# Optimization experiments

Measured on AMD Instinct MI355X. Metric: run time of the kernel, lower is better.

## Reference

```python
import jax, jax.numpy as jnp
import numpy as np

B, V, N, IN_F, HEADS, OUT_F = 4, 4, 1000, 64, 4, 32
D = HEADS * OUT_F  # 128, concat=True
E = 64000
NEG_SLOPE = 0.2


def setup_inputs() -> dict:
    key = jax.random.key(0)
    ks = jax.random.split(key, 8)
    x = jax.random.normal(ks[0], (B, V, N, IN_F), jnp.float32)
    edge_index = jax.random.randint(ks[1], (2, E), 0, B * N, dtype=jnp.int64)
    W = jax.random.normal(ks[2], (HEADS * OUT_F, IN_F), jnp.float32) / np.sqrt(IN_F)
    att = jax.random.normal(ks[3], (1, HEADS, 2 * OUT_F), jnp.float32) * 0.1
    in_proj_w = jax.random.normal(ks[4], (3 * D, D), jnp.float32) / np.sqrt(D)
    in_proj_b = jnp.zeros((3 * D,), jnp.float32)
    out_proj_w = jax.random.normal(ks[5], (D, D), jnp.float32) / np.sqrt(D)
    out_proj_b = jnp.zeros((D,), jnp.float32)
    bias = jnp.zeros((D,), jnp.float32)
    return dict(x=x, W=W, att=att, in_proj_w=in_proj_w, in_proj_b=in_proj_b,
                out_proj_w=out_proj_w, out_proj_b=out_proj_b, bias=bias,
                edge_index=edge_index)


def reference(x, W, att, in_proj_w, in_proj_b, out_proj_w, out_proj_b, bias, edge_index):
    Bx, Vx, Nx, _ = x.shape
    Ntot = Bx * Nx
    # intra-view GAT: shared W across views
    h = jnp.einsum('bvni,oi->bvno', x, W).reshape(Bx, Vx, Nx, HEADS, OUT_F)
    # block-diagonal placement: h_full[b*V+v, b*N:(b+1)*N] = h[b,v]
    ib = jnp.arange(Bx)
    hf = jnp.zeros((Bx, Vx, Bx, Nx, HEADS, OUT_F), x.dtype).at[ib, :, ib].set(h)
    h_full = hf.reshape(Bx * Vx, Ntot, HEADS, OUT_F)
    # add self loops
    loops = jnp.arange(Ntot, dtype=edge_index.dtype)
    src = jnp.concatenate([edge_index[0], loops])
    dst = jnp.concatenate([edge_index[1], loops])
    # attention scores (faithful to source: flatten h_full over (B*V, Ntot) and
    # index with raw node ids, i.e. gathers from block 0 only)
    h_flat = h_full.reshape(Bx * Vx * Ntot, HEADS, OUT_F)
    h_cat = jnp.concatenate([h_flat[src], h_flat[dst]], axis=-1)  # [Etot, H, 2*OUT]
    att_in = jax.nn.leaky_relu(h_cat, NEG_SLOPE)
    scores = jnp.sum(att * att_in, axis=-1)  # [Etot, HEADS]
    # per-destination segment softmax
    seg_max = jax.ops.segment_max(scores, dst, num_segments=Ntot)
    seg_max = jax.lax.stop_gradient(jnp.where(jnp.isfinite(seg_max), seg_max, 0.0))
    ex = jnp.exp(scores - seg_max[dst])
    denom = jax.ops.segment_sum(ex, dst, num_segments=Ntot)
    alpha = ex / (denom[dst] + 1e-16)  # [Etot, HEADS]
    # scatter-add aggregation, broadcast over B*V rows
    msgs = h_full[:, src] * alpha[None, :, :, None]  # [B*V, Etot, H, OUT]
    out_full = jnp.zeros_like(h_full).at[:, dst].add(msgs)
    # extract each graph's own node block
    out = out_full.reshape(Bx, Vx, Bx, Nx, HEADS, OUT_F)[ib, :, ib]  # [B,V,N,H,OUT]
    h_gat = out.reshape(Bx, Vx, Nx, HEADS * OUT_F)  # concat heads
    # inter-view mixing: MHA over the V axis per node
    seq = h_gat.transpose(0, 2, 1, 3).reshape(Bx * Nx, Vx, D)
    q, k, v = jnp.split(seq @ in_proj_w.T + in_proj_b, 3, axis=-1)
    hd = D // HEADS
    sp = lambda t: t.reshape(Bx * Nx, Vx, HEADS, hd).transpose(0, 2, 1, 3)
    q, k, v = sp(q), sp(k), sp(v)
    aw = jax.nn.softmax(jnp.einsum('bhqd,bhkd->bhqk', q, k) / jnp.sqrt(jnp.asarray(hd, x.dtype)), axis=-1)
    ao = jnp.einsum('bhqk,bhkd->bhqd', aw, v).transpose(0, 2, 1, 3).reshape(Bx * Nx, Vx, D)
    mixed = ao @ out_proj_w.T + out_proj_b
    h_mixed = mixed.reshape(Bx, Nx, Vx, D).transpose(0, 2, 1, 3)  # [B,V,N,D]
    return h_mixed + bias
```

## Files before the change

kernel.cpp:

```cpp
#include <hip/hip_runtime.h>

#define NN 1000
#define HEADS_ 4
#define DM 128
#define EE 64000
#define NTOT 4000
#define ETOT 68000
#define CAP 48
#define EB 34

template <int K, int SCORE, int REMAP>
__device__ void gemm_tile(int mi, int ni,
                          const float* __restrict__ A, const float* __restrict__ Wt,
                          const float* __restrict__ b1, const float* __restrict__ b2,
                          float* __restrict__ C, int N,
                          const float* __restrict__ att,
                          float* __restrict__ ssrc, float* __restrict__ sdst) {
  __shared__ float As[128 * 64];
  __shared__ float Bs[64 * 64];
  int tid = threadIdx.x;
  int m0 = mi * 128, n0 = ni * 64;
  int tx = tid & 15, ty = tid >> 4;
  const float4* A4 = (const float4*)A;
  const float4* W4 = (const float4*)Wt;
  float acc[8][4] = {};

  for (int c = 0; c < K / 64; ++c) {
    __syncthreads();
    {
      int q = tid & 15;
      int r0 = tid >> 4;
#pragma unroll
      for (int p = 0; p < 8; ++p) {
        int r = r0 + p * 16;
        float4 v = A4[(size_t)(m0 + r) * (K / 4) + c * 16 + q];
        *(float4*)&As[r * 64 + ((q ^ ((r >> 2) & 15)) << 2)] = v;
      }
#pragma unroll
      for (int p = 0; p < 4; ++p) {
        int r = r0 + p * 16;
        float4 v = W4[(size_t)(n0 + r) * (K / 4) + c * 16 + q];
        *(float4*)&Bs[r * 64 + ((q ^ ((r >> 2) & 15)) << 2)] = v;
      }
    }
    __syncthreads();
#pragma unroll 4
    for (int q = 0; q < 16; ++q) {
      float4 a[8], b[4];
#pragma unroll
      for (int i = 0; i < 8; ++i) {
        int r = ty * 8 + i;
        a[i] = *(const float4*)&As[r * 64 + ((q ^ ((r >> 2) & 15)) << 2)];
      }
#pragma unroll
      for (int j = 0; j < 4; ++j) {
        int rn = tx * 4 + j;
        b[j] = *(const float4*)&Bs[rn * 64 + ((q ^ ((rn >> 2) & 15)) << 2)];
      }
#pragma unroll
      for (int i = 0; i < 8; ++i)
#pragma unroll
        for (int j = 0; j < 4; ++j)
          acc[i][j] += a[i].x * b[j].x + a[i].y * b[j].y
                     + a[i].z * b[j].z + a[i].w * b[j].w;
    }
  }

  float bd[4] = {0.f, 0.f, 0.f, 0.f};
  int nc = n0 + tx * 4;
  if (b1) { bd[0] = b1[nc]; bd[1] = b1[nc+1]; bd[2] = b1[nc+2]; bd[3] = b1[nc+3]; }
  if (b2) { bd[0] += b2[nc]; bd[1] += b2[nc+1]; bd[2] += b2[nc+2]; bd[3] += b2[nc+3]; }
#pragma unroll
  for (int i = 0; i < 8; ++i) {
    int m = m0 + ty * 8 + i;
    int om = m;
    if (REMAP) {
      int node = m >> 2, v = m & 3;
      int b = node / NN, n = node - b * NN;
      om = (b * 4 + v) * NN + n;
    }
    float4 o = make_float4(acc[i][0] + bd[0], acc[i][1] + bd[1],
                           acc[i][2] + bd[2], acc[i][3] + bd[3]);
    *(float4*)&C[(size_t)om * N + nc] = o;
  }

  if (SCORE && m0 < NN) {
    int hsel = tx >> 3;
    int h = ni * 2 + hsel;
    int kb = (tx & 7) * 4;
    float a0[4], a1[4];
#pragma unroll
    for (int j = 0; j < 4; ++j) {
      a0[j] = att[h * 64 + kb + j];
      a1[j] = att[h * 64 + 32 + kb + j];
    }
#pragma unroll
    for (int i = 0; i < 8; ++i) {
      int m = m0 + ty * 8 + i;
      float p0 = 0.f, p1 = 0.f;
#pragma unroll
      for (int j = 0; j < 4; ++j) {
        float g = acc[i][j];
        float lr = g > 0.f ? g : 0.2f * g;
        p0 += a0[j] * lr;
        p1 += a1[j] * lr;
      }
      p0 += __shfl_xor(p0, 1, 16); p1 += __shfl_xor(p1, 1, 16);
      p0 += __shfl_xor(p0, 2, 16); p1 += __shfl_xor(p1, 2, 16);
      p0 += __shfl_xor(p0, 4, 16); p1 += __shfl_xor(p1, 4, 16);
      if ((tx & 7) == 0 && m < NN) {
        ssrc[m * HEADS_ + h] = p0;
        sdst[m * HEADS_ + h] = p1;
      }
    }
  }
}

__global__ __launch_bounds__(256) void k1_kernel(const float* __restrict__ x,
                                                 const float* __restrict__ W,
                                                 const float* __restrict__ att,
                                                 float* __restrict__ hbuf,
                                                 float* __restrict__ ssrc,
                                                 float* __restrict__ sdst,
                                                 const int* __restrict__ ei,
                                                 int* __restrict__ cnt,
                                                 int* __restrict__ elist) {
  int bid = blockIdx.x;
  if (bid < 250) {
    gemm_tile<64, 1, 0>(bid >> 1, bid & 1, x, W, nullptr, nullptr, hbuf, 128,
                        att, ssrc, sdst);
  } else {
    for (int e = (bid - 250) * 256 + threadIdx.x; e < ETOT; e += EB * 256) {
      int s, d;
      if (e < EE) { s = ei[e]; d = ei[EE + e]; }
      else { s = d = e - EE; }
      int pos = atomicAdd(&cnt[d], 1);
      if (pos < CAP) elist[d * CAP + pos] = s;
    }
  }
}

__global__ __launch_bounds__(256) void gather_kernel(const int* __restrict__ cnt,
                                                     const int* __restrict__ elist,
                                                     const float* __restrict__ ssrc,
                                                     const float* __restrict__ sdst,
                                                     const float* __restrict__ hbuf,
                                                     float* __restrict__ hgat) {
  __shared__ int   srcs[2][CAP];
  __shared__ float exs[2][CAP][HEADS_];
  int li = threadIdx.x >> 7;
  int t = threadIdx.x & 127;
  int d = blockIdx.x * 2 + li;
  int b = d / NN;
  int v = t >> 5, q = t & 31, h = q >> 3;
  int m = cnt[d]; if (m > CAP) m = CAP;
  for (int base = 0; base < m; base += 32) {
    int i = base + (t >> 2);
    if (i < m) {
      int s = elist[d * CAP + i];
      if ((t & 3) == 0) srcs[li][i] = s;
      float sc = ssrc[s * HEADS_ + (t & 3)] + sdst[d * HEADS_ + (t & 3)];
      exs[li][i][t & 3] = __expf(sc);
    }
  }
  __syncthreads();
  float den = 1e-16f;
  float4 acc = make_float4(0.f, 0.f, 0.f, 0.f);
  const float* hbase = hbuf + ((size_t)(b * 4 + v) * NN) * DM + q * 4;
  for (int i = 0; i < m; ++i) {
    float ex = exs[li][i][h];
    den += ex;
    unsigned sl = (unsigned)(srcs[li][i] - b * NN);
    if (sl < NN) {
      float4 hv = *(const float4*)(hbase + (size_t)sl * DM);
      acc.x += ex * hv.x; acc.y += ex * hv.y;
      acc.z += ex * hv.z; acc.w += ex * hv.w;
    }
  }
  float r = 1.f / den;
  acc.x *= r; acc.y *= r; acc.z *= r; acc.w *= r;
  *(float4*)&hgat[((size_t)(d * 4 + v)) * DM + q * 4] = acc;
}

__global__ __launch_bounds__(256) void qkv_kernel(const float* __restrict__ hgat,
                                                  const float* __restrict__ inw,
                                                  const float* __restrict__ inb,
                                                  float* __restrict__ qkv) {
  gemm_tile<128, 0, 0>(blockIdx.x, blockIdx.y, hgat, inw, inb, nullptr, qkv,
                       384, nullptr, nullptr, nullptr);
}

__global__ __launch_bounds__(256) void attn_kernel(const float* __restrict__ qkv,
                                                   float* __restrict__ ao) {
  int li = threadIdx.x >> 7;
  int t = threadIdx.x & 127;
  int node = blockIdx.x * 2 + li;
  __shared__ float qs[2][4][DM], ks[2][4][DM], vs[2][4][DM];
  __shared__ float aw[2][4][HEADS_][4];
#pragma unroll
  for (int v = 0; v < 4; ++v) {
    size_t base = (size_t)(node * 4 + v) * 384;
    qs[li][v][t] = qkv[base + t];
    ks[li][v][t] = qkv[base + 128 + t];
    vs[li][v][t] = qkv[base + 256 + t];
  }
  __syncthreads();
  if (t < 64) {
    int vq = t >> 4, vk = (t >> 2) & 3, h = t & 3;
    float acc = 0.f;
#pragma unroll
    for (int kd = 0; kd < 32; ++kd)
      acc += qs[li][vq][h * 32 + kd] * ks[li][vk][h * 32 + kd];
    aw[li][vq][h][vk] = acc * 0.17677669529663687f;
  }
  __syncthreads();
  if (t < 16) {
    int vq = t >> 2, h = t & 3;
    float mx = aw[li][vq][h][0];
    for (int i = 1; i < 4; ++i) mx = fmaxf(mx, aw[li][vq][h][i]);
    float e[4], s = 0.f;
    for (int i = 0; i < 4; ++i) { e[i] = __expf(aw[li][vq][h][i] - mx); s += e[i]; }
    for (int i = 0; i < 4; ++i) aw[li][vq][h][i] = e[i] / s;
  }
  __syncthreads();
  int h = t >> 5;
#pragma unroll
  for (int vq = 0; vq < 4; ++vq) {
    float acc = 0.f;
#pragma unroll
    for (int vk = 0; vk < 4; ++vk) acc += aw[li][vq][h][vk] * vs[li][vk][t];
    ao[(size_t)(node * 4 + vq) * DM + t] = acc;
  }
}

__global__ __launch_bounds__(256) void outproj_kernel(const float* __restrict__ ao,
                                                      const float* __restrict__ outw,
                                                      const float* __restrict__ outb,
                                                      const float* __restrict__ bias,
                                                      float* __restrict__ out) {
  gemm_tile<128, 0, 1>(blockIdx.x, blockIdx.y, ao, outw, outb, bias, out, 128,
                       nullptr, nullptr, nullptr);
}

extern "C" void kernel_launch(void* const* d_in, const int* in_sizes, int n_in,
                              void* d_out, int out_size, void* d_ws, size_t ws_size,
                              hipStream_t stream) {
  const float* x    = (const float*)d_in[0];
  const float* W    = (const float*)d_in[1];
  const float* att  = (const float*)d_in[2];
  const float* inw  = (const float*)d_in[3];
  const float* inb  = (const float*)d_in[4];
  const float* outw = (const float*)d_in[5];
  const float* outb = (const float*)d_in[6];
  const float* bias = (const float*)d_in[7];
  const int*   ei   = (const int*)d_in[8];
  float* out = (float*)d_out;

  float* ws = (float*)d_ws;
  float* hbuf  = ws;
  float* hgat  = ws + 2100000;
  float* qkv   = ws + 4200000;
  float* ao    = ws + 10400000;
  float* ssrc  = ws + 12500000;
  float* sdst  = ssrc + 16000;
  int*   cnt   = (int*)(sdst + 16000);
  int*   elist = cnt + 4000;

  hipMemsetAsync(ssrc, 0, 36000 * sizeof(float), stream);

  k1_kernel<<<250 + EB, 256, 0, stream>>>(x, W, att, hbuf, ssrc, sdst, ei, cnt, elist);
  gather_kernel<<<NTOT / 2, 256, 0, stream>>>(cnt, elist, ssrc, sdst, hbuf, hgat);
  qkv_kernel<<<dim3(125, 6), 256, 0, stream>>>(hgat, inw, inb, qkv);
  attn_kernel<<<NTOT / 2, 256, 0, stream>>>(qkv, ao);
  outproj_kernel<<<dim3(125, 2), 256, 0, stream>>>(ao, outw, outb, bias, out);
}
```

Baseline: 152.7 us.

## Fuse QKV projection, view attention and output projection into one kernel

Replaces the three kernels (QKV GEMM, per-node view attention, output projection) with a single kernel. Each block handles 16 nodes (64 rows) and keeps the QKV tile, attention weights and attention output in LDS, so the qkv and ao intermediates never go through global memory and two launches are removed. The cost is a large dynamic LDS allocation (about 149 KB, with an opt-in attribute) that limits occupancy to one block per CU. The grid is also only 250 blocks, each re-streaming the full projection weights.

```diff
diff --git a/kernel.cpp b/kernel.cpp
--- a/kernel.cpp
+++ b/kernel.cpp
@@ -9,10 +9,9 @@
 #define CAP 48
 #define EB 34
 
-template <int K, int SCORE, int REMAP>
+template <int K, int SCORE>
 __device__ void gemm_tile(int mi, int ni,
                           const float* __restrict__ A, const float* __restrict__ Wt,
-                          const float* __restrict__ b1, const float* __restrict__ b2,
                           float* __restrict__ C, int N,
                           const float* __restrict__ att,
                           float* __restrict__ ssrc, float* __restrict__ sdst) {
@@ -66,22 +65,12 @@
     }
   }
 
-  float bd[4] = {0.f, 0.f, 0.f, 0.f};
   int nc = n0 + tx * 4;
-  if (b1) { bd[0] = b1[nc]; bd[1] = b1[nc+1]; bd[2] = b1[nc+2]; bd[3] = b1[nc+3]; }
-  if (b2) { bd[0] += b2[nc]; bd[1] += b2[nc+1]; bd[2] += b2[nc+2]; bd[3] += b2[nc+3]; }
 #pragma unroll
   for (int i = 0; i < 8; ++i) {
     int m = m0 + ty * 8 + i;
-    int om = m;
-    if (REMAP) {
-      int node = m >> 2, v = m & 3;
-      int b = node / NN, n = node - b * NN;
-      om = (b * 4 + v) * NN + n;
-    }
-    float4 o = make_float4(acc[i][0] + bd[0], acc[i][1] + bd[1],
-                           acc[i][2] + bd[2], acc[i][3] + bd[3]);
-    *(float4*)&C[(size_t)om * N + nc] = o;
+    float4 o = make_float4(acc[i][0], acc[i][1], acc[i][2], acc[i][3]);
+    *(float4*)&C[(size_t)m * N + nc] = o;
   }
 
   if (SCORE && m0 < NN) {
@@ -127,8 +116,7 @@
                                                  int* __restrict__ elist) {
   int bid = blockIdx.x;
   if (bid < 250) {
-    gemm_tile<64, 1, 0>(bid >> 1, bid & 1, x, W, nullptr, nullptr, hbuf, 128,
-                        att, ssrc, sdst);
+    gemm_tile<64, 1>(bid >> 1, bid & 1, x, W, hbuf, 128, att, ssrc, sdst);
   } else {
     for (int e = (bid - 250) * 256 + threadIdx.x; e < ETOT; e += EB * 256) {
       int s, d;
@@ -182,64 +170,181 @@
   *(float4*)&hgat[((size_t)(d * 4 + v)) * DM + q * 4] = acc;
 }
 
-__global__ __launch_bounds__(256) void qkv_kernel(const float* __restrict__ hgat,
-                                                  const float* __restrict__ inw,
-                                                  const float* __restrict__ inb,
-                                                  float* __restrict__ qkv) {
-  gemm_tile<128, 0, 0>(blockIdx.x, blockIdx.y, hgat, inw, inb, nullptr, qkv,
-                       384, nullptr, nullptr, nullptr);
-}
-
-__global__ __launch_bounds__(256) void attn_kernel(const float* __restrict__ qkv,
-                                                   float* __restrict__ ao) {
-  int li = threadIdx.x >> 7;
-  int t = threadIdx.x & 127;
-  int node = blockIdx.x * 2 + li;
-  __shared__ float qs[2][4][DM], ks[2][4][DM], vs[2][4][DM];
-  __shared__ float aw[2][4][HEADS_][4];
-#pragma unroll
-  for (int v = 0; v < 4; ++v) {
-    size_t base = (size_t)(node * 4 + v) * 384;
-    qs[li][v][t] = qkv[base + t];
-    ks[li][v][t] = qkv[base + 128 + t];
-    vs[li][v][t] = qkv[base + 256 + t];
+#define QS 388
+
+__global__ __launch_bounds__(256) void fused3_kernel(const float* __restrict__ hgat,
+                                                     const float* __restrict__ inw,
+                                                     const float* __restrict__ inb,
+                                                     const float* __restrict__ outw,
+                                                     const float* __restrict__ outb,
+                                                     const float* __restrict__ bias,
+                                                     float* __restrict__ out) {
+  extern __shared__ float smem[];
+  float* As = smem;
+  float* Bs = smem + 8192;
+  float* qk = smem + 12288;
+  float* aw = smem + 37120;
+
+  int tid = threadIdx.x;
+  int g0 = blockIdx.x * 16;
+  int tx = tid & 15, ty = tid >> 4;
+
+  {
+    const float4* H4 = (const float4*)(hgat + (size_t)(g0 * 4) * DM);
+#pragma unroll
+    for (int p = 0; p < 8; ++p) {
+      int idx = p * 256 + tid;
+      int r = idx >> 5, qp = idx & 31;
+      float4 v = H4[idx];
+      int c = qp >> 4, q = qp & 15;
+      *(float4*)&As[c * 4096 + r * 64 + ((q ^ ((r >> 2) & 15)) << 2)] = v;
+    }
+  }
+
+  const float4* W4 = (const float4*)inw;
+  for (int ni = 0; ni < 6; ++ni) {
+    float acc[4][4] = {};
+    for (int c = 0; c < 2; ++c) {
+      __syncthreads();
+      {
+        int q = tid & 15, r0 = tid >> 4;
+#pragma unroll
+        for (int p = 0; p < 4; ++p) {
+          int r = r0 + p * 16;
+          float4 v = W4[(size_t)(ni * 64 + r) * 32 + c * 16 + q];
+          *(float4*)&Bs[r * 64 + ((q ^ ((r >> 2) & 15)) << 2)] = v;
+        }
+      }
+      __syncthreads();
+#pragma unroll 4
+      for (int q = 0; q < 16; ++q) {
+        float4 a[4], b[4];
+#pragma unroll
+        for (int i = 0; i < 4; ++i) {
+          int r = ty * 4 + i;
+          a[i] = *(const float4*)&As[c * 4096 + r * 64 + ((q ^ ((r >> 2) & 15)) << 2)];
+        }
+#pragma unroll
+        for (int j = 0; j < 4; ++j) {
+          int rn = tx * 4 + j;
+          b[j] = *(const float4*)&Bs[rn * 64 + ((q ^ ((rn >> 2) & 15)) << 2)];
+        }
+#pragma unroll
+        for (int i = 0; i < 4; ++i)
+#pragma unroll
+          for (int j = 0; j < 4; ++j)
+            acc[i][j] += a[i].x * b[j].x + a[i].y * b[j].y
+                       + a[i].z * b[j].z + a[i].w * b[j].w;
+      }
+    }
+    int nc = ni * 64 + tx * 4;
+    float b0 = inb[nc], b1 = inb[nc + 1], b2 = inb[nc + 2], b3 = inb[nc + 3];
+#pragma unroll
+    for (int i = 0; i < 4; ++i) {
+      int r = ty * 4 + i;
+      *(float4*)&qk[r * QS + nc] =
+          make_float4(acc[i][0] + b0, acc[i][1] + b1, acc[i][2] + b2, acc[i][3] + b3);
+    }
   }
   __syncthreads();
-  if (t < 64) {
-    int vq = t >> 4, vk = (t >> 2) & 3, h = t & 3;
-    float acc = 0.f;
-#pragma unroll
-    for (int kd = 0; kd < 32; ++kd)
-      acc += qs[li][vq][h * 32 + kd] * ks[li][vk][h * 32 + kd];
-    aw[li][vq][h][vk] = acc * 0.17677669529663687f;
+
+  {
+    int ln = tid >> 4, vq = (tid >> 2) & 3, h = tid & 3;
+    float4 qv[8];
+    const float* qr = &qk[(ln * 4 + vq) * QS + h * 32];
+#pragma unroll
+    for (int u = 0; u < 8; ++u) qv[u] = *(const float4*)&qr[u * 4];
+    float sc[4];
+#pragma unroll
+    for (int vk = 0; vk < 4; ++vk) {
+      const float* kr = &qk[(ln * 4 + vk) * QS + 128 + h * 32];
+      float s = 0.f;
+#pragma unroll
+      for (int u = 0; u < 8; ++u) {
+        float4 kv = *(const float4*)&kr[u * 4];
+        s += qv[u].x * kv.x + qv[u].y * kv.y + qv[u].z * kv.z + qv[u].w * kv.w;
+      }
+      sc[vk] = s * 0.17677669529663687f;
+    }
+    float mx = fmaxf(fmaxf(sc[0], sc[1]), fmaxf(sc[2], sc[3]));
+    float e0 = __expf(sc[0] - mx), e1 = __expf(sc[1] - mx);
+    float e2 = __expf(sc[2] - mx), e3 = __expf(sc[3] - mx);
+    float inv = 1.f / (e0 + e1 + e2 + e3);
+    aw[tid * 4 + 0] = e0 * inv; aw[tid * 4 + 1] = e1 * inv;
+    aw[tid * 4 + 2] = e2 * inv; aw[tid * 4 + 3] = e3 * inv;
   }
   __syncthreads();
-  if (t < 16) {
-    int vq = t >> 2, h = t & 3;
-    float mx = aw[li][vq][h][0];
-    for (int i = 1; i < 4; ++i) mx = fmaxf(mx, aw[li][vq][h][i]);
-    float e[4], s = 0.f;
-    for (int i = 0; i < 4; ++i) { e[i] = __expf(aw[li][vq][h][i] - mx); s += e[i]; }
-    for (int i = 0; i < 4; ++i) aw[li][vq][h][i] = e[i] / s;
-  }
-  __syncthreads();
-  int h = t >> 5;
-#pragma unroll
-  for (int vq = 0; vq < 4; ++vq) {
-    float acc = 0.f;
-#pragma unroll
-    for (int vk = 0; vk < 4; ++vk) acc += aw[li][vq][h][vk] * vs[li][vk][t];
-    ao[(size_t)(node * 4 + vq) * DM + t] = acc;
-  }
-}
-
-__global__ __launch_bounds__(256) void outproj_kernel(const float* __restrict__ ao,
-                                                      const float* __restrict__ outw,
-                                                      const float* __restrict__ outb,
-                                                      const float* __restrict__ bias,
-                                                      float* __restrict__ out) {
-  gemm_tile<128, 0, 1>(blockIdx.x, blockIdx.y, ao, outw, outb, bias, out, 128,
-                       nullptr, nullptr, nullptr);
+
+  {
+    int ln = tid >> 4, rem = tid & 15, vq = rem >> 2, h = rem & 3;
+    float wv[4];
+#pragma unroll
+    for (int vk = 0; vk < 4; ++vk)
+      wv[vk] = aw[((ln << 4) + (vq << 2) + h) * 4 + vk];
+    int r = ln * 4 + vq;
+#pragma unroll
+    for (int u = 0; u < 8; ++u) {
+      float4 a4 = make_float4(0.f, 0.f, 0.f, 0.f);
+#pragma unroll
+      for (int vk = 0; vk < 4; ++vk) {
+        float4 vv = *(const float4*)&qk[(ln * 4 + vk) * QS + 256 + h * 32 + u * 4];
+        a4.x += wv[vk] * vv.x; a4.y += wv[vk] * vv.y;
+        a4.z += wv[vk] * vv.z; a4.w += wv[vk] * vv.w;
+      }
+      int qp = h * 8 + u, c = qp >> 4, q = qp & 15;
+      *(float4*)&As[c * 4096 + r * 64 + ((q ^ ((r >> 2) & 15)) << 2)] = a4;
+    }
+  }
+
+  const float4* O4 = (const float4*)outw;
+  for (int ni = 0; ni < 2; ++ni) {
+    float acc[4][4] = {};
+    for (int c = 0; c < 2; ++c) {
+      __syncthreads();
+      {
+        int q = tid & 15, r0 = tid >> 4;
+#pragma unroll
+        for (int p = 0; p < 4; ++p) {
+          int r = r0 + p * 16;
+          float4 v = O4[(size_t)(ni * 64 + r) * 32 + c * 16 + q];
+          *(float4*)&Bs[r * 64 + ((q ^ ((r >> 2) & 15)) << 2)] = v;
+        }
+      }
+      __syncthreads();
+#pragma unroll 4
+      for (int q = 0; q < 16; ++q) {
+        float4 a[4], b[4];
+#pragma unroll
+        for (int i = 0; i < 4; ++i) {
+          int r = ty * 4 + i;
+          a[i] = *(const float4*)&As[c * 4096 + r * 64 + ((q ^ ((r >> 2) & 15)) << 2)];
+        }
+#pragma unroll
+        for (int j = 0; j < 4; ++j) {
+          int rn = tx * 4 + j;
+          b[j] = *(const float4*)&Bs[rn * 64 + ((q ^ ((rn >> 2) & 15)) << 2)];
+        }
+#pragma unroll
+        for (int i = 0; i < 4; ++i)
+#pragma unroll
+          for (int j = 0; j < 4; ++j)
+            acc[i][j] += a[i].x * b[j].x + a[i].y * b[j].y
+                       + a[i].z * b[j].z + a[i].w * b[j].w;
+      }
+    }
+    int nc = ni * 64 + tx * 4;
+    float b0 = outb[nc] + bias[nc], b1 = outb[nc + 1] + bias[nc + 1];
+    float b2 = outb[nc + 2] + bias[nc + 2], b3 = outb[nc + 3] + bias[nc + 3];
+#pragma unroll
+    for (int i = 0; i < 4; ++i) {
+      int r = ty * 4 + i;
+      int g = g0 + (r >> 2), v = r & 3;
+      int bg = g / NN, n = g - bg * NN;
+      int om = (bg * 4 + v) * NN + n;
+      *(float4*)&out[(size_t)om * DM + nc] =
+          make_float4(acc[i][0] + b0, acc[i][1] + b1, acc[i][2] + b2, acc[i][3] + b3);
+    }
+  }
 }
 
 extern "C" void kernel_launch(void* const* d_in, const int* in_sizes, int n_in,
@@ -259,18 +364,21 @@
   float* ws = (float*)d_ws;
   float* hbuf  = ws;
   float* hgat  = ws + 2100000;
-  float* qkv   = ws + 4200000;
-  float* ao    = ws + 10400000;
   float* ssrc  = ws + 12500000;
   float* sdst  = ssrc + 16000;
   int*   cnt   = (int*)(sdst + 16000);
   int*   elist = cnt + 4000;
 
+  static int lds_opt_in = 0;
+  if (!lds_opt_in) {
+    hipFuncSetAttribute((const void*)fused3_kernel,
+                        hipFuncAttributeMaxDynamicSharedMemorySize, 160 * 1024);
+    lds_opt_in = 1;
+  }
+
   hipMemsetAsync(ssrc, 0, 36000 * sizeof(float), stream);
 
   k1_kernel<<<250 + EB, 256, 0, stream>>>(x, W, att, hbuf, ssrc, sdst, ei, cnt, elist);
   gather_kernel<<<NTOT / 2, 256, 0, stream>>>(cnt, elist, ssrc, sdst, hbuf, hgat);
-  qkv_kernel<<<dim3(125, 6), 256, 0, stream>>>(hgat, inw, inb, qkv);
-  attn_kernel<<<NTOT / 2, 256, 0, stream>>>(qkv, ao);
-  outproj_kernel<<<dim3(125, 2), 256, 0, stream>>>(ao, outw, outb, bias, out);
-}
+  fused3_kernel<<<250, 256, 152576, stream>>>(hgat, inw, inb, outw, outb, bias, out);
+}
```

Result: slower. 162.4 us (+6.4%).
